# Kernel optimization log

Hardware: AMD Instinct MI355X
Metric: run time of the kernel (lower is better)

Reference implementation:

```python
import jax, jax.numpy as jnp
import numpy as np

TEMPERATURE = 1.0          # max(args.matching_temperature=1.0, 1e-6)
CONSISTENCY_WEIGHT = 0.5   # max(args.matching_consistency_weight=0.5, 0.0)
EPS = 1e-6

N, M, D, K = 16384, 16384, 128, 5


def setup_inputs() -> dict:
    key = jax.random.key(0)
    k1, k2, k3 = jax.random.split(key, 3)
    query = jax.random.normal(k1, (N, D), dtype=jnp.float32)
    memory_bank = jax.random.normal(k2, (M, D), dtype=jnp.float32)
    # per-memory-entry neighbor scale (positive), as in _build_patch_library_statistics
    neighbor_scale_bank = jax.random.uniform(k3, (M,), dtype=jnp.float32) + 0.1
    return {"query": query, "memory_bank": memory_bank,
            "neighbor_scale_bank": neighbor_scale_bank, "k": K}


def reference(query, memory_bank, neighbor_scale_bank, k):
    # Euclidean cdist: [N, M]
    q2 = jnp.sum(query * query, axis=-1, keepdims=True)            # [N,1]
    m2 = jnp.sum(memory_bank * memory_bank, axis=-1)               # [M]
    d2 = q2 + m2 - 2.0 * (query @ memory_bank.T)                   # [N,M]
    dist = jnp.sqrt(jnp.maximum(d2, 1e-12))

    # torch.topk(largest=False) -> k smallest distances, ascending
    neg_d, knn_indices = jax.lax.top_k(-dist, k)                   # [N,k]
    knn_distances = -neg_d

    # adaptive_knn reduction (_reduce_knn_distances)
    weights = jax.nn.softmax(-knn_distances / TEMPERATURE, axis=1)
    weighted_distance = jnp.sum(weights * knn_distances, axis=1)   # [N]

    neighbor_scale = jnp.mean(neighbor_scale_bank[knn_indices], axis=1)  # [N]
    normalized_distance = weighted_distance / jnp.maximum(neighbor_scale, EPS)

    mean_d = jnp.mean(knn_distances, axis=1)
    std_d = jnp.sqrt(jnp.maximum(
        jnp.mean((knn_distances - mean_d[:, None]) ** 2, axis=1), 0.0))  # unbiased=False
    consistency = std_d / jnp.maximum(mean_d, EPS)

    return normalized_distance * (1.0 + CONSISTENCY_WEIGHT * consistency)
```

## Files before the change

### kernel.cpp

```cpp
#include <hip/hip_runtime.h>
#include <hip/hip_bf16.h>
#include <math.h>

#define N_Q 16384
#define N_M 16384
#define DIM 128
#define KNN 5
#define SPLITS 8
#define COLS_PER_SPLIT (N_M / SPLITS)
#define ITERS (COLS_PER_SPLIT / 128)
#define BROWS 256
#define TSEL 8
#define TSEL2 16
#define LLIST 4
#define BIGF 3.0e38f

typedef __bf16 bf16x8 __attribute__((ext_vector_type(8)));
typedef float f32x4 __attribute__((ext_vector_type(4)));

__device__ __forceinline__ void gl2lds16(const void* g, void* l) {
    __builtin_amdgcn_global_load_lds(
        (const __attribute__((address_space(1))) void*)g,
        (__attribute__((address_space(3))) void*)l, 16, 0, 0);
}

__device__ __forceinline__ unsigned umed3(unsigned a, unsigned b, unsigned c) {
    unsigned d;
    asm("v_med3_u32 %0, %1, %2, %3" : "=v"(d) : "v"(a), "v"(b), "v"(c));
    return d;
}

template <int D>
__device__ __forceinline__ void insD(unsigned (&L)[D], unsigned k) {
#pragma unroll
    for (int i = D - 1; i >= 1; --i) L[i] = umed3(L[i - 1], L[i], k);
    L[0] = min(L[0], k);
}

__global__ void prep_kernel(const float* __restrict__ q,
                            const float* __restrict__ mem,
                            float* __restrict__ q2, float* __restrict__ m2,
                            float* __restrict__ m2b,
                            __hip_bfloat16* __restrict__ qb,
                            __hip_bfloat16* __restrict__ mb) {
    int gt = blockIdx.x * blockDim.x + threadIdx.x;
    int wid = gt >> 6;
    int lane = gt & 63;
    bool isq = wid < N_Q;
    int r = isq ? wid : wid - N_Q;
    const float* src = (isq ? q : mem) + (size_t)r * DIM;
    __hip_bfloat16* bdst = (isq ? qb : mb) + (size_t)r * DIM;
    float2 v = reinterpret_cast<const float2*>(src)[lane];
    float sc = isq ? 1.0f : -2.0f;
    __hip_bfloat162 bv;
    bv.x = __float2bfloat16(sc * v.x);
    bv.y = __float2bfloat16(sc * v.y);
    reinterpret_cast<__hip_bfloat162*>(bdst)[lane] = bv;
    float s = fmaf(v.x, v.x, v.y * v.y);
#pragma unroll
    for (int off = 32; off > 0; off >>= 1) s += __shfl_down(s, off, 64);
    if (lane == 0) {
        if (isq) {
            q2[r] = s;
        } else {
            m2[r] = s;
            m2b[r] = s + 256.0f;
        }
    }
}

__global__ __launch_bounds__(256, 2) void knn_tops_kernel(
    const __hip_bfloat16* __restrict__ qb, const __hip_bfloat16* __restrict__ mb,
    const float* __restrict__ m2b, unsigned* __restrict__ candK) {
    __shared__ __align__(16) unsigned char smem[33792];
    const int tid = threadIdx.x;
    const int w = tid >> 6;
    const int lane = tid & 63;
    const int i16 = lane & 15;
    const int g = lane >> 4;
    const int row0 = blockIdx.x * BROWS;
    const int col0 = blockIdx.y * COLS_PER_SPLIT;

    bf16x8 afrag[4][4];
#pragma unroll
    for (int ti = 0; ti < 4; ++ti) {
        const __hip_bfloat16* qrow =
            qb + (size_t)(row0 + w * 64 + ti * 16 + i16) * DIM;
#pragma unroll
        for (int ks = 0; ks < 4; ++ks)
            afrag[ti][ks] = *reinterpret_cast<const bf16x8*>(qrow + ks * 32 + g * 8);
    }

    unsigned lst[16][LLIST];
#pragma unroll
    for (int rr = 0; rr < 16; ++rr)
#pragma unroll
        for (int j = 0; j < LLIST; ++j) lst[rr][j] = 0xFFFFFFFFu;

    const int lds_base = i16 * 256 + ((g ^ (i16 & 7)) << 4);
    int soff[8];
#pragma unroll
    for (int it = 0; it < 8; ++it) {
        int fg = w * 512 + it * 64 + lane;
        int c = fg >> 4, sg = fg & 15;
        int gk = (sg & 8) | ((sg ^ c) & 7);
        soff[it] = c * DIM + gk * 8;
    }
    const __hip_bfloat16* mbt = mb + (size_t)col0 * DIM;

    for (int t = 0; t < ITERS; ++t) {
        __syncthreads();
#pragma unroll
        for (int it = 0; it < 8; ++it)
            gl2lds16(mbt + soff[it], smem + w * 8192 + it * 1024);
        mbt += 128 * DIM;
        __syncthreads();

        float m2r[8];
        unsigned colv[8];
#pragma unroll
        for (int h = 0; h < 2; ++h)
#pragma unroll
            for (int c = 0; c < 4; ++c) {
                int cl = col0 + t * 128 + h * 64 + c * 16 + i16;
                m2r[h * 4 + c] = m2b[cl];
                colv[h * 4 + c] = (unsigned)cl;
            }
#pragma unroll
        for (int half = 0; half < 2; ++half) {
#pragma unroll
            for (int cc = 0; cc < 2; ++cc) {
                f32x4 acc[4][2];
#pragma unroll
                for (int ti = 0; ti < 4; ++ti)
#pragma unroll
                    for (int c2 = 0; c2 < 2; ++c2) {
                        float m = m2r[half * 4 + cc * 2 + c2];
                        acc[ti][c2] = (f32x4){m, m, m, m};
                    }
#pragma unroll
                for (int ks = 0; ks < 4; ++ks) {
                    const unsigned char* bp =
                        smem + (lds_base ^ (ks << 6)) + half * 16384;
#pragma unroll
                    for (int c2 = 0; c2 < 2; ++c2) {
                        int ct = cc * 2 + c2;
                        bf16x8 bfr =
                            *reinterpret_cast<const bf16x8*>(bp + ct * 4096);
#pragma unroll
                        for (int ti = 0; ti < 4; ++ti)
                            acc[ti][c2] = __builtin_amdgcn_mfma_f32_16x16x32_bf16(
                                afrag[ti][ks], bfr, acc[ti][c2], 0, 0, 0);
                    }
                }
#pragma unroll
                for (int ti = 0; ti < 4; ++ti) {
#pragma unroll
                    for (int r = 0; r < 4; ++r) {
                        const int rr = ti * 4 + r;
#pragma unroll
                        for (int c2 = 0; c2 < 2; ++c2) {
                            unsigned k = (__float_as_uint(acc[ti][c2][r]) &
                                          0xFFFFC000u) |
                                         colv[half * 4 + cc * 2 + c2];
                            insD(lst[rr], k);
                        }
                    }
                }
            }
        }
    }

    __syncthreads();

#pragma unroll
    for (int rr = 0; rr < 16; ++rr) {
        unsigned pv[LLIST];
#pragma unroll
        for (int j = 0; j < LLIST; ++j)
            pv[j] = (unsigned)__shfl_xor((int)lst[rr][j], 8, 64);
#pragma unroll
        for (int j = 0; j < LLIST; ++j) insD(lst[rr], pv[j]);
    }
    unsigned* MG = (unsigned*)smem;
    if (i16 < 8) {
#pragma unroll
        for (int rr = 0; rr < 16; ++rr) {
            int row = w * 64 + (rr >> 2) * 16 + g * 4 + (rr & 3);
#pragma unroll
            for (int j = 0; j < LLIST; ++j)
                MG[row * 33 + i16 * LLIST + j] = lst[rr][j];
        }
    }
    __syncthreads();
    {
        unsigned bk[TSEL];
#pragma unroll
        for (int j = 0; j < TSEL; ++j) bk[j] = 0xFFFFFFFFu;
        for (int c = 0; c < 32; ++c) {
            unsigned k = MG[tid * 33 + c];
            insD(bk, k);
        }
        size_t base = (size_t)(row0 + tid) * (SPLITS * TSEL) + blockIdx.y * TSEL;
        *reinterpret_cast<uint4*>(candK + base) =
            make_uint4(bk[0], bk[1], bk[2], bk[3]);
        *reinterpret_cast<uint4*>(candK + base + 4) =
            make_uint4(bk[4], bk[5], bk[6], bk[7]);
    }
}

__global__ void merge_kernel(const unsigned* __restrict__ candK,
                             int* __restrict__ candI2) {
    int row = blockIdx.x * blockDim.x + threadIdx.x;
    const unsigned* ck = candK + (size_t)row * (SPLITS * TSEL);
    unsigned v[TSEL2];
#pragma unroll
    for (int j = 0; j < TSEL2; ++j) v[j] = 0xFFFFFFFFu;
    for (int s4 = 0; s4 < 16; ++s4) {
        uint4 kk = reinterpret_cast<const uint4*>(ck)[s4];
        insD(v, kk.x);
        insD(v, kk.y);
        insD(v, kk.z);
        insD(v, kk.w);
    }
#pragma unroll
    for (int j = 0; j < TSEL2; ++j)
        candI2[(size_t)row * TSEL2 + j] = (int)(v[j] & 0x3FFFu);
}

__global__ __launch_bounds__(256) void finalize_kernel(
    const float* __restrict__ q, const float* __restrict__ mem,
    const float* __restrict__ q2, const float* __restrict__ m2,
    const int* __restrict__ candI2, const float* __restrict__ scaleb,
    float* __restrict__ out) {
    int wv = threadIdx.x >> 6, lane = threadIdx.x & 63;
    int n = blockIdx.x * 4 + wv;
    int cand = lane >> 2, qd = lane & 3;
    int ci = candI2[(size_t)n * TSEL2 + cand];
    const float4* qr = reinterpret_cast<const float4*>(q + (size_t)n * DIM) + qd * 8;
    const float4* mr = reinterpret_cast<const float4*>(mem + (size_t)ci * DIM) + qd * 8;
    float dot = 0.f;
#pragma unroll
    for (int k = 0; k < 8; ++k) {
        float4 a = qr[k], b = mr[k];
        dot = fmaf(a.x, b.x, fmaf(a.y, b.y, fmaf(a.z, b.z, fmaf(a.w, b.w, dot))));
    }
    dot += __shfl_xor(dot, 1, 64);
    dot += __shfl_xor(dot, 2, 64);
    float v = (qd == 0) ? (q2[n] + m2[ci] - 2.f * dot) : BIGF;

    float dk[KNN]; int ik[KNN];
#pragma unroll
    for (int r = 0; r < KNN; ++r) {
        float mv = v; int ml = lane;
#pragma unroll
        for (int off = 32; off > 0; off >>= 1) {
            float ov = __shfl_xor(mv, off, 64);
            int   ol = __shfl_xor(ml, off, 64);
            if (ov < mv || (ov == mv && ol < ml)) { mv = ov; ml = ol; }
        }
        dk[r] = sqrtf(fmaxf(mv, 1e-12f));
        ik[r] = __shfl(ci, ml, 64);
        if (lane == ml) v = BIGF;
    }
    if (lane == 0) {
        float dmin = dk[0];
        float se = 0.f, wd = 0.f, sm = 0.f, ssc = 0.f;
#pragma unroll
        for (int j = 0; j < KNN; ++j) {
            float e = expf(-(dk[j] - dmin));
            se += e;
            wd = fmaf(e, dk[j], wd);
            sm += dk[j];
            ssc += scaleb[ik[j]];
        }
        wd /= se;
        float scale = ssc * 0.2f;
        float nd = wd / fmaxf(scale, 1e-6f);
        float mean = sm * 0.2f;
        float var = 0.f;
#pragma unroll
        for (int j = 0; j < KNN; ++j) {
            float dd = dk[j] - mean;
            var = fmaf(dd, dd, var);
        }
        var *= 0.2f;
        float cons = sqrtf(var) / fmaxf(mean, 1e-6f);
        out[n] = nd * (1.f + 0.5f * cons);
    }
}

extern "C" void kernel_launch(void* const* d_in, const int* in_sizes, int n_in,
                              void* d_out, int out_size, void* d_ws,
                              size_t ws_size, hipStream_t stream) {
    const float* query  = (const float*)d_in[0];
    const float* mem    = (const float*)d_in[1];
    const float* scaleb = (const float*)d_in[2];
    float* out = (float*)d_out;

    float* q2 = (float*)d_ws;
    float* m2 = q2 + N_Q;
    float* m2b = m2 + N_M;
    __hip_bfloat16* qb = (__hip_bfloat16*)(m2b + N_M);
    __hip_bfloat16* mb = qb + (size_t)N_Q * DIM;
    unsigned* candK = (unsigned*)(mb + (size_t)N_M * DIM);
    int* candI2 = (int*)(candK + (size_t)N_Q * SPLITS * TSEL);

    prep_kernel<<<(N_Q + N_M) / 4, 256, 0, stream>>>(query, mem, q2, m2, m2b,
                                                     qb, mb);
    dim3 gridB(N_Q / BROWS, SPLITS);
    knn_tops_kernel<<<gridB, 256, 0, stream>>>(qb, mb, m2b, candK);
    merge_kernel<<<N_Q / 256, 256, 0, stream>>>(candK, candI2);
    finalize_kernel<<<N_Q / 4, 256, 0, stream>>>(query, mem, q2, m2, candI2,
                                                 scaleb, out);
}
```

Measured before the change: 200.5 us.

## Convert query to bf16 in-kernel, double column splits, compute exact diff distance

Query vectors are now cast from fp32 to bf16 inside the top-k GEMM kernel, so the prep kernel no longer converts them or computes q2. Column splits go from 8 to 16, doubling grid parallelism but also doubling candidate storage and the number of entries the merge kernel scans. Finalize now computes the squared difference directly instead of the q2+m2-2dot expansion, which drops the norm buffers. The trade is more merge work and candidate traffic in exchange for more blocks in flight and a lighter prep pass.

```diff
diff --git a/kernel.cpp b/kernel.cpp
--- a/kernel.cpp
+++ b/kernel.cpp
@@ -6,7 +6,7 @@
 #define N_M 16384
 #define DIM 128
 #define KNN 5
-#define SPLITS 8
+#define SPLITS 16
 #define COLS_PER_SPLIT (N_M / SPLITS)
 #define ITERS (COLS_PER_SPLIT / 128)
 #define BROWS 256
@@ -37,40 +37,26 @@
     L[0] = min(L[0], k);
 }
 
-__global__ void prep_kernel(const float* __restrict__ q,
-                            const float* __restrict__ mem,
-                            float* __restrict__ q2, float* __restrict__ m2,
+__global__ void prep_kernel(const float* __restrict__ mem,
                             float* __restrict__ m2b,
-                            __hip_bfloat16* __restrict__ qb,
                             __hip_bfloat16* __restrict__ mb) {
     int gt = blockIdx.x * blockDim.x + threadIdx.x;
     int wid = gt >> 6;
     int lane = gt & 63;
-    bool isq = wid < N_Q;
-    int r = isq ? wid : wid - N_Q;
-    const float* src = (isq ? q : mem) + (size_t)r * DIM;
-    __hip_bfloat16* bdst = (isq ? qb : mb) + (size_t)r * DIM;
+    const float* src = mem + (size_t)wid * DIM;
     float2 v = reinterpret_cast<const float2*>(src)[lane];
-    float sc = isq ? 1.0f : -2.0f;
     __hip_bfloat162 bv;
-    bv.x = __float2bfloat16(sc * v.x);
-    bv.y = __float2bfloat16(sc * v.y);
-    reinterpret_cast<__hip_bfloat162*>(bdst)[lane] = bv;
+    bv.x = __float2bfloat16(-2.f * v.x);
+    bv.y = __float2bfloat16(-2.f * v.y);
+    reinterpret_cast<__hip_bfloat162*>(mb + (size_t)wid * DIM)[lane] = bv;
     float s = fmaf(v.x, v.x, v.y * v.y);
 #pragma unroll
     for (int off = 32; off > 0; off >>= 1) s += __shfl_down(s, off, 64);
-    if (lane == 0) {
-        if (isq) {
-            q2[r] = s;
-        } else {
-            m2[r] = s;
-            m2b[r] = s + 256.0f;
-        }
-    }
+    if (lane == 0) m2b[wid] = s + 256.0f;
 }
 
 __global__ __launch_bounds__(256, 2) void knn_tops_kernel(
-    const __hip_bfloat16* __restrict__ qb, const __hip_bfloat16* __restrict__ mb,
+    const float* __restrict__ qf, const __hip_bfloat16* __restrict__ mb,
     const float* __restrict__ m2b, unsigned* __restrict__ candK) {
     __shared__ __align__(16) unsigned char smem[33792];
     const int tid = threadIdx.x;
@@ -84,11 +70,19 @@
     bf16x8 afrag[4][4];
 #pragma unroll
     for (int ti = 0; ti < 4; ++ti) {
-        const __hip_bfloat16* qrow =
-            qb + (size_t)(row0 + w * 64 + ti * 16 + i16) * DIM;
-#pragma unroll
-        for (int ks = 0; ks < 4; ++ks)
-            afrag[ti][ks] = *reinterpret_cast<const bf16x8*>(qrow + ks * 32 + g * 8);
+        const float* qrow = qf + (size_t)(row0 + w * 64 + ti * 16 + i16) * DIM;
+#pragma unroll
+        for (int ks = 0; ks < 4; ++ks) {
+            const float4* p =
+                reinterpret_cast<const float4*>(qrow + ks * 32 + g * 8);
+            float4 a0 = p[0], a1 = p[1];
+            bf16x8 f;
+            f[0] = (__bf16)a0.x; f[1] = (__bf16)a0.y;
+            f[2] = (__bf16)a0.z; f[3] = (__bf16)a0.w;
+            f[4] = (__bf16)a1.x; f[5] = (__bf16)a1.y;
+            f[6] = (__bf16)a1.z; f[7] = (__bf16)a1.w;
+            afrag[ti][ks] = f;
+        }
     }
 
     unsigned lst[16][LLIST];
@@ -216,7 +210,7 @@
     unsigned v[TSEL2];
 #pragma unroll
     for (int j = 0; j < TSEL2; ++j) v[j] = 0xFFFFFFFFu;
-    for (int s4 = 0; s4 < 16; ++s4) {
+    for (int s4 = 0; s4 < (SPLITS * TSEL) / 4; ++s4) {
         uint4 kk = reinterpret_cast<const uint4*>(ck)[s4];
         insD(v, kk.x);
         insD(v, kk.y);
@@ -230,7 +224,6 @@
 
 __global__ __launch_bounds__(256) void finalize_kernel(
     const float* __restrict__ q, const float* __restrict__ mem,
-    const float* __restrict__ q2, const float* __restrict__ m2,
     const int* __restrict__ candI2, const float* __restrict__ scaleb,
     float* __restrict__ out) {
     int wv = threadIdx.x >> 6, lane = threadIdx.x & 63;
@@ -239,15 +232,19 @@
     int ci = candI2[(size_t)n * TSEL2 + cand];
     const float4* qr = reinterpret_cast<const float4*>(q + (size_t)n * DIM) + qd * 8;
     const float4* mr = reinterpret_cast<const float4*>(mem + (size_t)ci * DIM) + qd * 8;
-    float dot = 0.f;
+    float d2 = 0.f;
 #pragma unroll
     for (int k = 0; k < 8; ++k) {
         float4 a = qr[k], b = mr[k];
-        dot = fmaf(a.x, b.x, fmaf(a.y, b.y, fmaf(a.z, b.z, fmaf(a.w, b.w, dot))));
-    }
-    dot += __shfl_xor(dot, 1, 64);
-    dot += __shfl_xor(dot, 2, 64);
-    float v = (qd == 0) ? (q2[n] + m2[ci] - 2.f * dot) : BIGF;
+        float dx = a.x - b.x, dy = a.y - b.y, dz = a.z - b.z, dw = a.w - b.w;
+        d2 = fmaf(dx, dx, d2);
+        d2 = fmaf(dy, dy, d2);
+        d2 = fmaf(dz, dz, d2);
+        d2 = fmaf(dw, dw, d2);
+    }
+    d2 += __shfl_xor(d2, 1, 64);
+    d2 += __shfl_xor(d2, 2, 64);
+    float v = (qd == 0) ? d2 : BIGF;
 
     float dk[KNN]; int ik[KNN];
 #pragma unroll
@@ -298,19 +295,15 @@
     const float* scaleb = (const float*)d_in[2];
     float* out = (float*)d_out;
 
-    float* q2 = (float*)d_ws;
-    float* m2 = q2 + N_Q;
-    float* m2b = m2 + N_M;
-    __hip_bfloat16* qb = (__hip_bfloat16*)(m2b + N_M);
-    __hip_bfloat16* mb = qb + (size_t)N_Q * DIM;
+    float* m2b = (float*)d_ws;
+    __hip_bfloat16* mb = (__hip_bfloat16*)(m2b + N_M);
     unsigned* candK = (unsigned*)(mb + (size_t)N_M * DIM);
     int* candI2 = (int*)(candK + (size_t)N_Q * SPLITS * TSEL);
 
-    prep_kernel<<<(N_Q + N_M) / 4, 256, 0, stream>>>(query, mem, q2, m2, m2b,
-                                                     qb, mb);
+    prep_kernel<<<N_M / 4, 256, 0, stream>>>(mem, m2b, mb);
     dim3 gridB(N_Q / BROWS, SPLITS);
-    knn_tops_kernel<<<gridB, 256, 0, stream>>>(qb, mb, m2b, candK);
+    knn_tops_kernel<<<gridB, 256, 0, stream>>>(query, mb, m2b, candK);
     merge_kernel<<<N_Q / 256, 256, 0, stream>>>(candK, candI2);
-    finalize_kernel<<<N_Q / 4, 256, 0, stream>>>(query, mem, q2, m2, candI2,
-                                                 scaleb, out);
-}
+    finalize_kernel<<<N_Q / 4, 256, 0, stream>>>(query, mem, candI2, scaleb,
+                                                 out);
+}
```

Measured after the change: 211.8 us. 1.06x slower.

## Double KNN column tile and fuse candidate merge into finalize kernel

Applied to the files above, without the earlier changes.

The main kNN kernel now stages 256 memory columns per iteration instead of 128, using 64 KB of LDS. This halves the number of barrier/load rounds but may lower occupancy. The separate merge kernel is folded into finalize, where 64 threads per block merge candidates into shared memory before the refinement. Finalize now computes exact squared distances directly, so the q2/m2 norm computation and buffers are dropped. This removes one launch and some global traffic.

```diff
diff --git a/kernel.cpp b/kernel.cpp
--- a/kernel.cpp
+++ b/kernel.cpp
@@ -8,7 +8,8 @@
 #define KNN 5
 #define SPLITS 8
 #define COLS_PER_SPLIT (N_M / SPLITS)
-#define ITERS (COLS_PER_SPLIT / 128)
+#define TILE_COLS 256
+#define ITERS (COLS_PER_SPLIT / TILE_COLS)
 #define BROWS 256
 #define TSEL 8
 #define TSEL2 16
@@ -39,7 +40,6 @@
 
 __global__ void prep_kernel(const float* __restrict__ q,
                             const float* __restrict__ mem,
-                            float* __restrict__ q2, float* __restrict__ m2,
                             float* __restrict__ m2b,
                             __hip_bfloat16* __restrict__ qb,
                             __hip_bfloat16* __restrict__ mb) {
@@ -56,23 +56,18 @@
     bv.x = __float2bfloat16(sc * v.x);
     bv.y = __float2bfloat16(sc * v.y);
     reinterpret_cast<__hip_bfloat162*>(bdst)[lane] = bv;
-    float s = fmaf(v.x, v.x, v.y * v.y);
-#pragma unroll
-    for (int off = 32; off > 0; off >>= 1) s += __shfl_down(s, off, 64);
-    if (lane == 0) {
-        if (isq) {
-            q2[r] = s;
-        } else {
-            m2[r] = s;
-            m2b[r] = s + 256.0f;
-        }
+    if (!isq) {
+        float s = fmaf(v.x, v.x, v.y * v.y);
+#pragma unroll
+        for (int off = 32; off > 0; off >>= 1) s += __shfl_down(s, off, 64);
+        if (lane == 0) m2b[r] = s + 256.0f;
     }
 }
 
 __global__ __launch_bounds__(256, 2) void knn_tops_kernel(
     const __hip_bfloat16* __restrict__ qb, const __hip_bfloat16* __restrict__ mb,
     const float* __restrict__ m2b, unsigned* __restrict__ candK) {
-    __shared__ __align__(16) unsigned char smem[33792];
+    __shared__ __align__(16) unsigned char smem[65536];
     const int tid = threadIdx.x;
     const int w = tid >> 6;
     const int lane = tid & 63;
@@ -98,10 +93,10 @@
         for (int j = 0; j < LLIST; ++j) lst[rr][j] = 0xFFFFFFFFu;
 
     const int lds_base = i16 * 256 + ((g ^ (i16 & 7)) << 4);
-    int soff[8];
-#pragma unroll
-    for (int it = 0; it < 8; ++it) {
-        int fg = w * 512 + it * 64 + lane;
+    int soff[16];
+#pragma unroll
+    for (int it = 0; it < 16; ++it) {
+        int fg = w * 1024 + it * 64 + lane;
         int c = fg >> 4, sg = fg & 15;
         int gk = (sg & 8) | ((sg ^ c) & 7);
         soff[it] = c * DIM + gk * 8;
@@ -111,60 +106,52 @@
     for (int t = 0; t < ITERS; ++t) {
         __syncthreads();
 #pragma unroll
-        for (int it = 0; it < 8; ++it)
-            gl2lds16(mbt + soff[it], smem + w * 8192 + it * 1024);
-        mbt += 128 * DIM;
+        for (int it = 0; it < 16; ++it)
+            gl2lds16(mbt + soff[it], smem + w * 16384 + it * 1024);
+        mbt += TILE_COLS * DIM;
         __syncthreads();
 
-        float m2r[8];
-        unsigned colv[8];
-#pragma unroll
-        for (int h = 0; h < 2; ++h)
-#pragma unroll
-            for (int c = 0; c < 4; ++c) {
-                int cl = col0 + t * 128 + h * 64 + c * 16 + i16;
-                m2r[h * 4 + c] = m2b[cl];
-                colv[h * 4 + c] = (unsigned)cl;
-            }
-#pragma unroll
-        for (int half = 0; half < 2; ++half) {
-#pragma unroll
-            for (int cc = 0; cc < 2; ++cc) {
-                f32x4 acc[4][2];
-#pragma unroll
-                for (int ti = 0; ti < 4; ++ti)
+        float m2r[16];
+#pragma unroll
+        for (int c = 0; c < 16; ++c)
+            m2r[c] = m2b[col0 + t * TILE_COLS + c * 16 + i16];
+        const unsigned colb = (unsigned)(col0 + t * TILE_COLS + i16);
+
+#pragma unroll
+        for (int cc = 0; cc < 8; ++cc) {
+            f32x4 acc[4][2];
+#pragma unroll
+            for (int ti = 0; ti < 4; ++ti)
+#pragma unroll
+                for (int c2 = 0; c2 < 2; ++c2) {
+                    float m = m2r[cc * 2 + c2];
+                    acc[ti][c2] = (f32x4){m, m, m, m};
+                }
+#pragma unroll
+            for (int ks = 0; ks < 4; ++ks) {
+                const unsigned char* bp = smem + (lds_base ^ (ks << 6));
+#pragma unroll
+                for (int c2 = 0; c2 < 2; ++c2) {
+                    int ct = cc * 2 + c2;
+                    bf16x8 bfr =
+                        *reinterpret_cast<const bf16x8*>(bp + ct * 4096);
+#pragma unroll
+                    for (int ti = 0; ti < 4; ++ti)
+                        acc[ti][c2] = __builtin_amdgcn_mfma_f32_16x16x32_bf16(
+                            afrag[ti][ks], bfr, acc[ti][c2], 0, 0, 0);
+                }
+            }
+#pragma unroll
+            for (int ti = 0; ti < 4; ++ti) {
+#pragma unroll
+                for (int r = 0; r < 4; ++r) {
+                    const int rr = ti * 4 + r;
 #pragma unroll
                     for (int c2 = 0; c2 < 2; ++c2) {
-                        float m = m2r[half * 4 + cc * 2 + c2];
-                        acc[ti][c2] = (f32x4){m, m, m, m};
-                    }
-#pragma unroll
-                for (int ks = 0; ks < 4; ++ks) {
-                    const unsigned char* bp =
-                        smem + (lds_base ^ (ks << 6)) + half * 16384;
-#pragma unroll
-                    for (int c2 = 0; c2 < 2; ++c2) {
-                        int ct = cc * 2 + c2;
-                        bf16x8 bfr =
-                            *reinterpret_cast<const bf16x8*>(bp + ct * 4096);
-#pragma unroll
-                        for (int ti = 0; ti < 4; ++ti)
-                            acc[ti][c2] = __builtin_amdgcn_mfma_f32_16x16x32_bf16(
-                                afrag[ti][ks], bfr, acc[ti][c2], 0, 0, 0);
-                    }
-                }
-#pragma unroll
-                for (int ti = 0; ti < 4; ++ti) {
-#pragma unroll
-                    for (int r = 0; r < 4; ++r) {
-                        const int rr = ti * 4 + r;
-#pragma unroll
-                        for (int c2 = 0; c2 < 2; ++c2) {
-                            unsigned k = (__float_as_uint(acc[ti][c2][r]) &
-                                          0xFFFFC000u) |
-                                         colv[half * 4 + cc * 2 + c2];
-                            insD(lst[rr], k);
-                        }
+                        unsigned k = (__float_as_uint(acc[ti][c2][r]) &
+                                      0xFFFFC000u) |
+                                     (colb + (cc * 2 + c2) * 16);
+                        insD(lst[rr], k);
                     }
                 }
             }
@@ -209,84 +196,96 @@
     }
 }
 
-__global__ void merge_kernel(const unsigned* __restrict__ candK,
-                             int* __restrict__ candI2) {
-    int row = blockIdx.x * blockDim.x + threadIdx.x;
-    const unsigned* ck = candK + (size_t)row * (SPLITS * TSEL);
-    unsigned v[TSEL2];
-#pragma unroll
-    for (int j = 0; j < TSEL2; ++j) v[j] = 0xFFFFFFFFu;
-    for (int s4 = 0; s4 < 16; ++s4) {
-        uint4 kk = reinterpret_cast<const uint4*>(ck)[s4];
-        insD(v, kk.x);
-        insD(v, kk.y);
-        insD(v, kk.z);
-        insD(v, kk.w);
-    }
-#pragma unroll
-    for (int j = 0; j < TSEL2; ++j)
-        candI2[(size_t)row * TSEL2 + j] = (int)(v[j] & 0x3FFFu);
-}
-
 __global__ __launch_bounds__(256) void finalize_kernel(
     const float* __restrict__ q, const float* __restrict__ mem,
-    const float* __restrict__ q2, const float* __restrict__ m2,
-    const int* __restrict__ candI2, const float* __restrict__ scaleb,
+    const unsigned* __restrict__ candK, const float* __restrict__ scaleb,
     float* __restrict__ out) {
-    int wv = threadIdx.x >> 6, lane = threadIdx.x & 63;
-    int n = blockIdx.x * 4 + wv;
-    int cand = lane >> 2, qd = lane & 3;
-    int ci = candI2[(size_t)n * TSEL2 + cand];
-    const float4* qr = reinterpret_cast<const float4*>(q + (size_t)n * DIM) + qd * 8;
-    const float4* mr = reinterpret_cast<const float4*>(mem + (size_t)ci * DIM) + qd * 8;
-    float dot = 0.f;
-#pragma unroll
-    for (int k = 0; k < 8; ++k) {
-        float4 a = qr[k], b = mr[k];
-        dot = fmaf(a.x, b.x, fmaf(a.y, b.y, fmaf(a.z, b.z, fmaf(a.w, b.w, dot))));
-    }
-    dot += __shfl_xor(dot, 1, 64);
-    dot += __shfl_xor(dot, 2, 64);
-    float v = (qd == 0) ? (q2[n] + m2[ci] - 2.f * dot) : BIGF;
-
-    float dk[KNN]; int ik[KNN];
-#pragma unroll
-    for (int r = 0; r < KNN; ++r) {
-        float mv = v; int ml = lane;
-#pragma unroll
-        for (int off = 32; off > 0; off >>= 1) {
-            float ov = __shfl_xor(mv, off, 64);
-            int   ol = __shfl_xor(ml, off, 64);
-            if (ov < mv || (ov == mv && ol < ml)) { mv = ov; ml = ol; }
-        }
-        dk[r] = sqrtf(fmaxf(mv, 1e-12f));
-        ik[r] = __shfl(ci, ml, 64);
-        if (lane == ml) v = BIGF;
-    }
-    if (lane == 0) {
-        float dmin = dk[0];
-        float se = 0.f, wd = 0.f, sm = 0.f, ssc = 0.f;
-#pragma unroll
-        for (int j = 0; j < KNN; ++j) {
-            float e = expf(-(dk[j] - dmin));
-            se += e;
-            wd = fmaf(e, dk[j], wd);
-            sm += dk[j];
-            ssc += scaleb[ik[j]];
-        }
-        wd /= se;
-        float scale = ssc * 0.2f;
-        float nd = wd / fmaxf(scale, 1e-6f);
-        float mean = sm * 0.2f;
-        float var = 0.f;
-#pragma unroll
-        for (int j = 0; j < KNN; ++j) {
-            float dd = dk[j] - mean;
-            var = fmaf(dd, dd, var);
-        }
-        var *= 0.2f;
-        float cons = sqrtf(var) / fmaxf(mean, 1e-6f);
-        out[n] = nd * (1.f + 0.5f * cons);
+    __shared__ int candS[64 * TSEL2];
+    const int tid = threadIdx.x;
+    const int n0 = blockIdx.x * 64;
+
+    if (tid < 64) {
+        const unsigned* ck = candK + (size_t)(n0 + tid) * (SPLITS * TSEL);
+        unsigned v[TSEL2];
+#pragma unroll
+        for (int j = 0; j < TSEL2; ++j) v[j] = 0xFFFFFFFFu;
+        for (int s4 = 0; s4 < (SPLITS * TSEL) / 4; ++s4) {
+            uint4 kk = reinterpret_cast<const uint4*>(ck)[s4];
+            insD(v, kk.x);
+            insD(v, kk.y);
+            insD(v, kk.z);
+            insD(v, kk.w);
+        }
+#pragma unroll
+        for (int j = 0; j < TSEL2; ++j)
+            candS[tid * TSEL2 + j] = (int)(v[j] & 0x3FFFu);
+    }
+    __syncthreads();
+
+    const int wv = tid >> 6, lane = tid & 63;
+    const int cand = lane >> 2, qd = lane & 3;
+    for (int i = 0; i < 16; ++i) {
+        const int qi = wv * 16 + i;
+        const int n = n0 + qi;
+        int ci = candS[qi * TSEL2 + cand];
+        const float4* qr =
+            reinterpret_cast<const float4*>(q + (size_t)n * DIM) + qd * 8;
+        const float4* mr =
+            reinterpret_cast<const float4*>(mem + (size_t)ci * DIM) + qd * 8;
+        float d2 = 0.f;
+#pragma unroll
+        for (int k = 0; k < 8; ++k) {
+            float4 a = qr[k], b = mr[k];
+            float dx = a.x - b.x, dy = a.y - b.y;
+            float dz = a.z - b.z, dw = a.w - b.w;
+            d2 = fmaf(dx, dx, d2);
+            d2 = fmaf(dy, dy, d2);
+            d2 = fmaf(dz, dz, d2);
+            d2 = fmaf(dw, dw, d2);
+        }
+        d2 += __shfl_xor(d2, 1, 64);
+        d2 += __shfl_xor(d2, 2, 64);
+        float v = (qd == 0) ? d2 : BIGF;
+
+        float dk[KNN]; int ik[KNN];
+#pragma unroll
+        for (int r = 0; r < KNN; ++r) {
+            float mv = v; int ml = lane;
+#pragma unroll
+            for (int off = 32; off > 0; off >>= 1) {
+                float ov = __shfl_xor(mv, off, 64);
+                int   ol = __shfl_xor(ml, off, 64);
+                if (ov < mv || (ov == mv && ol < ml)) { mv = ov; ml = ol; }
+            }
+            dk[r] = sqrtf(fmaxf(mv, 1e-12f));
+            ik[r] = __shfl(ci, ml, 64);
+            if (lane == ml) v = BIGF;
+        }
+        if (lane == 0) {
+            float dmin = dk[0];
+            float se = 0.f, wd = 0.f, sm = 0.f, ssc = 0.f;
+#pragma unroll
+            for (int j = 0; j < KNN; ++j) {
+                float e = expf(-(dk[j] - dmin));
+                se += e;
+                wd = fmaf(e, dk[j], wd);
+                sm += dk[j];
+                ssc += scaleb[ik[j]];
+            }
+            wd /= se;
+            float scale = ssc * 0.2f;
+            float nd = wd / fmaxf(scale, 1e-6f);
+            float mean = sm * 0.2f;
+            float var = 0.f;
+#pragma unroll
+            for (int j = 0; j < KNN; ++j) {
+                float dd = dk[j] - mean;
+                var = fmaf(dd, dd, var);
+            }
+            var *= 0.2f;
+            float cons = sqrtf(var) / fmaxf(mean, 1e-6f);
+            out[n] = nd * (1.f + 0.5f * cons);
+        }
     }
 }
 
@@ -298,19 +297,14 @@
     const float* scaleb = (const float*)d_in[2];
     float* out = (float*)d_out;
 
-    float* q2 = (float*)d_ws;
-    float* m2 = q2 + N_Q;
-    float* m2b = m2 + N_M;
+    float* m2b = (float*)d_ws;
     __hip_bfloat16* qb = (__hip_bfloat16*)(m2b + N_M);
     __hip_bfloat16* mb = qb + (size_t)N_Q * DIM;
     unsigned* candK = (unsigned*)(mb + (size_t)N_M * DIM);
-    int* candI2 = (int*)(candK + (size_t)N_Q * SPLITS * TSEL);
-
-    prep_kernel<<<(N_Q + N_M) / 4, 256, 0, stream>>>(query, mem, q2, m2, m2b,
-                                                     qb, mb);
+
+    prep_kernel<<<(N_Q + N_M) / 4, 256, 0, stream>>>(query, mem, m2b, qb, mb);
     dim3 gridB(N_Q / BROWS, SPLITS);
     knn_tops_kernel<<<gridB, 256, 0, stream>>>(qb, mb, m2b, candK);
-    merge_kernel<<<N_Q / 256, 256, 0, stream>>>(candK, candI2);
-    finalize_kernel<<<N_Q / 4, 256, 0, stream>>>(query, mem, q2, m2, candI2,
-                                                 scaleb, out);
-}
+    finalize_kernel<<<N_Q / 64, 256, 0, stream>>>(query, mem, candK, scaleb,
+                                                  out);
+}
```

After: 239.5 us. 1.19x slower.
